# Kernel optimization log

Hardware: AMD Instinct MI355X
Metric: run time of the kernel (lower is better)

The kernel has to match this reference:

```python
import jax, jax.numpy as jnp
import numpy as np
from jax import lax

INPUT, HIDDEN, LAYERS = 256, 512, 3
SEQ, BATCH = 1024, 32
STDV = 1.0 / float(np.sqrt(HIDDEN))


def _uniform(key, shape):
    return jax.random.uniform(key, shape, jnp.float32, -STDV, STDV)


def setup_inputs() -> dict:
    key = jax.random.key(0)
    ks = iter(jax.random.split(key, 64))
    x = jax.random.normal(next(ks), (SEQ, BATCH, INPUT), jnp.float32)
    H3 = 3 * HIDDEN
    # layer 0: input dim = INPUT; layers 1..2: input dim = 2*HIDDEN
    w_ih_l0 = _uniform(next(ks), (2, H3, INPUT))          # (dir, 3H, in)
    w_hh_l0 = _uniform(next(ks), (2, H3, HIDDEN))
    b_ih_l0 = _uniform(next(ks), (2, H3))
    b_hh_l0 = _uniform(next(ks), (2, H3))
    w_ih_lr = _uniform(next(ks), (LAYERS - 1, 2, H3, 2 * HIDDEN))
    w_hh_lr = _uniform(next(ks), (LAYERS - 1, 2, H3, HIDDEN))
    b_ih_lr = _uniform(next(ks), (LAYERS - 1, 2, H3))
    b_hh_lr = _uniform(next(ks), (LAYERS - 1, 2, H3))
    return dict(x=x, w_ih_l0=w_ih_l0, w_hh_l0=w_hh_l0, b_ih_l0=b_ih_l0,
                b_hh_l0=b_hh_l0, w_ih_lr=w_ih_lr, w_hh_lr=w_hh_lr,
                b_ih_lr=b_ih_lr, b_hh_lr=b_hh_lr)


def _gru_dir(xs, w_ih, w_hh, b_ih, b_hh, reverse):
    # xs: (T, B, in); precompute input projection for the whole sequence
    Xi = jnp.einsum('tbi,gi->tbg', xs, w_ih) + b_ih  # (T, B, 3H)
    h0 = jnp.zeros((xs.shape[1], HIDDEN), xs.dtype)

    def step(h, xi):
        hp = h @ w_hh.T + b_hh                       # (B, 3H)
        ir, iz, inn = jnp.split(xi, 3, axis=-1)
        hr, hz, hn = jnp.split(hp, 3, axis=-1)
        r = jax.nn.sigmoid(ir + hr)
        z = jax.nn.sigmoid(iz + hz)
        n = jnp.tanh(inn + r * hn)
        h_new = (1.0 - z) * n + z * h
        return h_new, h_new

    h_last, ys = lax.scan(step, h0, Xi, reverse=reverse)
    return h_last, ys  # ys in original time order even when reverse=True


def reference(x, w_ih_l0, w_hh_l0, b_ih_l0, b_hh_l0,
              w_ih_lr, w_hh_lr, b_ih_lr, b_hh_lr):
    layer_input = x
    h_n = []
    for layer in range(LAYERS):
        if layer == 0:
            wi, wh, bi, bh = w_ih_l0, w_hh_l0, b_ih_l0, b_hh_l0
        else:
            wi, wh = w_ih_lr[layer - 1], w_hh_lr[layer - 1]
            bi, bh = b_ih_lr[layer - 1], b_hh_lr[layer - 1]
        hf, yf = _gru_dir(layer_input, wi[0], wh[0], bi[0], bh[0], reverse=False)
        hb, yb = _gru_dir(layer_input, wi[1], wh[1], bi[1], bh[1], reverse=True)
        h_n.append(hf)
        h_n.append(hb)
        layer_input = jnp.concatenate([yf, yb], axis=-1)  # (T, B, 2H)
    return jnp.stack(h_n, axis=0)  # (LAYERS*2, B, H)
```

## Files before the change

### kernel.cpp

```cpp
#include <hip/hip_runtime.h>
#include <stdint.h>

#define SEQ   1024
#define BATCH 32
#define HID   512
#define G3    1536
#define NW    32
#define JPW   16
#define THREADS 384
#define FSTR  256
#define CSTR  64
#define CH    16
#define NCH   64
#define NG    192
#define NPROD 192

typedef __attribute__((ext_vector_type(8))) short  short8;
typedef __attribute__((ext_vector_type(4))) float  f32x4;
typedef __attribute__((ext_vector_type(4))) unsigned short us4;
typedef unsigned long long ull;

__device__ __forceinline__ unsigned short f2bf(float f) {
  union { float f; unsigned int u; } v; v.f = f;
  unsigned int u = v.u;
  return (unsigned short)((u + 0x7FFFu + ((u >> 16) & 1u)) >> 16);
}
__device__ __forceinline__ float bf2f(unsigned short u) {
  union { unsigned int i; float f; } v; v.i = ((unsigned int)u) << 16; return v.f;
}
__device__ __forceinline__ short8 pack8(const float* __restrict__ p) {
  short8 o;
#pragma unroll
  for (int i = 0; i < 8; i++) o[i] = (short)f2bf(p[i]);
  return o;
}

__global__ void cvt_wb(const float* __restrict__ w, short8* __restrict__ out, int kcx, int nc) {
  int c = blockIdx.x * blockDim.x + threadIdx.x;
  if (c >= nc) return;
  int lane = c & 63, r = c >> 6;
  int kc = r % kcx, ng = r / kcx;
  int n   = ng * 16 + (lane & 15);
  int col = kc * 32 + (lane >> 4) * 8;
  int K = kcx * 32;
  out[c] = pack8(w + (size_t)n * K + col);
}

template<int KCX, bool WRITE_Y>
__global__ __launch_bounds__(THREADS, 1) void gru_mega(
    const void* __restrict__ Ain,
    short8* __restrict__ yout,
    const short8* __restrict__ wb,
    const float* __restrict__ whh,
    const float* __restrict__ bih,
    const float* __restrict__ bhh,
    us4* __restrict__ Xic,
    short8* __restrict__ hbuf,
    int* __restrict__ flags,
    int* __restrict__ prodcnt,
    float* __restrict__ hout)
{
  __shared__ float gbuf[4 * 512];
  __shared__ float hold[512];

  const int tid  = threadIdx.x;
  const int lane = tid & 63;
  const int wave = tid >> 6;
  const int quad = lane >> 4;
  const int l15  = lane & 15;

  if (blockIdx.x >= 64) {
    const int p    = blockIdx.x - 64;
    const int tg   = p & 15;
    const int ngg  = p >> 4;
    const int dirp = (ngg >= 6) ? 1 : 0;
    int* fl = flags + dirp * NW * FSTR;

    for (int c = 0; c < NCH; c++) {
      const int tgt = (c >= 2) ? CH * (c - 1) : 0;
      if (wave == 0) {
        while (true) {
          int v = (lane < NW)
                    ? __hip_atomic_load(&fl[lane * FSTR], __ATOMIC_RELAXED, __HIP_MEMORY_SCOPE_AGENT)
                    : tgt;
          if (__all(v >= tgt)) break;
          __builtin_amdgcn_s_sleep(4);
        }
      }
      __syncthreads();
      const int sl = tg;
      const int s  = c * CH + sl;
      const int t  = dirp ? (SEQ - 1 - s) : s;
      for (int mi = 0; mi < 2; mi++) {
        short8 a[KCX];
        if constexpr (KCX == 8) {
          const float* xr = (const float*)Ain + ((size_t)t * 32 + mi * 16 + l15) * 256 + quad * 8;
#pragma unroll
          for (int kc = 0; kc < KCX; kc++) a[kc] = pack8(xr + kc * 32);
        } else {
          const short8* ap = (const short8*)Ain + ((size_t)(t * 2 + mi) * KCX) * 64 + lane;
#pragma unroll
          for (int kc = 0; kc < KCX; kc++) a[kc] = ap[kc * 64];
        }
        for (int ng = ngg * 16 + wave; ng < ngg * 16 + 16; ng += 6) {
          const short8* bp = wb + (size_t)ng * KCX * 64 + lane;
          f32x4 ac0 = (f32x4){0.f, 0.f, 0.f, 0.f};
          f32x4 ac1 = (f32x4){0.f, 0.f, 0.f, 0.f};
#pragma unroll
          for (int kc = 0; kc < KCX; kc += 2) {
            ac0 = __builtin_amdgcn_mfma_f32_16x16x32_bf16(a[kc],     bp[kc * 64],       ac0, 0, 0, 0);
            ac1 = __builtin_amdgcn_mfma_f32_16x16x32_bf16(a[kc + 1], bp[(kc + 1) * 64], ac1, 0, 0, 0);
          }
          const int n  = ng * 16 + l15;
          const int gg = (ng % 96) >> 5;
          const float bias = bih[n] + (gg < 2 ? bhh[n] : 0.f);
          us4 o;
#pragma unroll
          for (int r = 0; r < 4; r++) o[r] = f2bf(ac0[r] + ac1[r] + bias);
          us4* dst = Xic + ((((size_t)(c & 1)) * CH + sl) * NG + ng) * 128 + mi * 64 + lane;
          asm volatile("global_store_dwordx2 %0, %1, off sc0 sc1" :: "v"(dst), "v"(o) : "memory");
        }
      }
      asm volatile("s_waitcnt vmcnt(0)" ::: "memory");
      __syncthreads();
      if (tid == 0)
        __hip_atomic_fetch_add(&prodcnt[c * CSTR], 1, __ATOMIC_RELAXED, __HIP_MEMORY_SCOPE_AGENT);
    }
    return;
  }

  const int mi  = wave & 1;
  const int g   = wave >> 1;
  const int dir = blockIdx.x >> 5;
  const int wg  = blockIdx.x & 31;
  const int j0  = wg * JPW;
  const bool rev = (dir == 1);
  const int ngR = dir * 96 + g * 32 + wg;

  short8 wh[16];
  {
    const float* pw = whh + (size_t)dir * G3 * HID + (size_t)(g * HID + j0 + l15) * HID + quad * 8;
#pragma unroll
    for (int kc = 0; kc < 16; kc++) wh[kc] = pack8(pw + kc * 32);
  }
  const float bh = bhh[dir * G3 + g * HID + j0 + l15];

  for (int idx = tid; idx < 512; idx += THREADS) hold[idx] = 0.f;
  __syncthreads();

  int* fl = flags + dir * NW * FSTR;
  char* hb = (char*)(hbuf + (size_t)dir * 2 * 2048);

  for (int s = 0; s < SEQ; s++) {
    const int t  = rev ? (SEQ - 1 - s) : s;
    const int c  = s >> 4;
    const int sl = s & 15;

    if (wave == 0) {
      while (true) {
        int v = (s > 0 && lane < NW)
                  ? __hip_atomic_load(&fl[lane * FSTR], __ATOMIC_RELAXED, __HIP_MEMORY_SCOPE_AGENT)
                  : s;
        bool ok = __all(v >= s);
        if (ok && sl == 0) {
          int cnt = __hip_atomic_load(&prodcnt[c * CSTR], __ATOMIC_RELAXED, __HIP_MEMORY_SCOPE_AGENT);
          ok = (cnt >= NPROD);
        }
        if (ok) break;
        __builtin_amdgcn_s_sleep(1);
      }
    }
    __syncthreads();

    const char* xp = (const char*)Xic
        + (((((size_t)(c & 1)) * CH + sl) * NG + ngR) * 128 + mi * 64 + lane) * 8;
    ull xi64;
    f32x4 p0 = (f32x4){0.f, 0.f, 0.f, 0.f};
    f32x4 p1 = (f32x4){0.f, 0.f, 0.f, 0.f};

    if (s > 0) {
      const char* hp = hb + (size_t)((s - 1) & 1) * 32768 + (size_t)mi * 16384 + (size_t)lane * 16;
      short8 a0, a1, a2, a3, a4, a5, a6, a7, a8, a9, a10, a11, a12, a13, a14, a15;
      asm volatile(
          "global_load_dwordx2 %16, %21, off sc0 sc1\n\t"
          "global_load_dwordx4 %0, %17, off sc0 sc1\n\t"
          "global_load_dwordx4 %1, %17, off offset:1024 sc0 sc1\n\t"
          "global_load_dwordx4 %2, %17, off offset:2048 sc0 sc1\n\t"
          "global_load_dwordx4 %3, %17, off offset:3072 sc0 sc1\n\t"
          "global_load_dwordx4 %4, %18, off sc0 sc1\n\t"
          "global_load_dwordx4 %5, %18, off offset:1024 sc0 sc1\n\t"
          "global_load_dwordx4 %6, %18, off offset:2048 sc0 sc1\n\t"
          "global_load_dwordx4 %7, %18, off offset:3072 sc0 sc1\n\t"
          "global_load_dwordx4 %8, %19, off sc0 sc1\n\t"
          "global_load_dwordx4 %9, %19, off offset:1024 sc0 sc1\n\t"
          "global_load_dwordx4 %10, %19, off offset:2048 sc0 sc1\n\t"
          "global_load_dwordx4 %11, %19, off offset:3072 sc0 sc1\n\t"
          "global_load_dwordx4 %12, %20, off sc0 sc1\n\t"
          "global_load_dwordx4 %13, %20, off offset:1024 sc0 sc1\n\t"
          "global_load_dwordx4 %14, %20, off offset:2048 sc0 sc1\n\t"
          "global_load_dwordx4 %15, %20, off offset:3072 sc0 sc1\n\t"
          "s_waitcnt vmcnt(0)"
          : "=&v"(a0), "=&v"(a1), "=&v"(a2), "=&v"(a3),
            "=&v"(a4), "=&v"(a5), "=&v"(a6), "=&v"(a7),
            "=&v"(a8), "=&v"(a9), "=&v"(a10), "=&v"(a11),
            "=&v"(a12), "=&v"(a13), "=&v"(a14), "=&v"(a15), "=&v"(xi64)
          : "v"(hp), "v"(hp + 4096), "v"(hp + 8192), "v"(hp + 12288), "v"(xp)
          : "memory");
      p0 = __builtin_amdgcn_mfma_f32_16x16x32_bf16(a0,  wh[0],  p0, 0, 0, 0);
      p1 = __builtin_amdgcn_mfma_f32_16x16x32_bf16(a1,  wh[1],  p1, 0, 0, 0);
      p0 = __builtin_amdgcn_mfma_f32_16x16x32_bf16(a2,  wh[2],  p0, 0, 0, 0);
      p1 = __builtin_amdgcn_mfma_f32_16x16x32_bf16(a3,  wh[3],  p1, 0, 0, 0);
      p0 = __builtin_amdgcn_mfma_f32_16x16x32_bf16(a4,  wh[4],  p0, 0, 0, 0);
      p1 = __builtin_amdgcn_mfma_f32_16x16x32_bf16(a5,  wh[5],  p1, 0, 0, 0);
      p0 = __builtin_amdgcn_mfma_f32_16x16x32_bf16(a6,  wh[6],  p0, 0, 0, 0);
      p1 = __builtin_amdgcn_mfma_f32_16x16x32_bf16(a7,  wh[7],  p1, 0, 0, 0);
      p0 = __builtin_amdgcn_mfma_f32_16x16x32_bf16(a8,  wh[8],  p0, 0, 0, 0);
      p1 = __builtin_amdgcn_mfma_f32_16x16x32_bf16(a9,  wh[9],  p1, 0, 0, 0);
      p0 = __builtin_amdgcn_mfma_f32_16x16x32_bf16(a10, wh[10], p0, 0, 0, 0);
      p1 = __builtin_amdgcn_mfma_f32_16x16x32_bf16(a11, wh[11], p1, 0, 0, 0);
      p0 = __builtin_amdgcn_mfma_f32_16x16x32_bf16(a12, wh[12], p0, 0, 0, 0);
      p1 = __builtin_amdgcn_mfma_f32_16x16x32_bf16(a13, wh[13], p1, 0, 0, 0);
      p0 = __builtin_amdgcn_mfma_f32_16x16x32_bf16(a14, wh[14], p0, 0, 0, 0);
      p1 = __builtin_amdgcn_mfma_f32_16x16x32_bf16(a15, wh[15], p1, 0, 0, 0);
    } else {
      asm volatile("global_load_dwordx2 %0, %1, off sc0 sc1\n\ts_waitcnt vmcnt(0)"
                   : "=&v"(xi64) : "v"(xp) : "memory");
    }

#pragma unroll
    for (int r = 0; r < 4; r++) {
      int m = mi * 16 + quad * 4 + r;
      float xv = bf2f((unsigned short)(xi64 >> (16 * r)));
      if (g < 2) {
        gbuf[(g * 32 + m) * JPW + l15] = xv + p0[r] + p1[r];
      } else {
        gbuf[(2 * 32 + m) * JPW + l15] = xv;
        gbuf[(3 * 32 + m) * JPW + l15] = bh + p0[r] + p1[r];
      }
    }
    __syncthreads();

    if (tid < 256) {
      int b = tid >> 3, jj = tid & 7;
      int e0 = b * 16 + 2 * jj;
      float h2[2];
#pragma unroll
      for (int e = 0; e < 2; e++) {
        int idx = e0 + e;
        int j = (idx & 15);
        float pr = gbuf[(0 * 32 + b) * JPW + j];
        float pz = gbuf[(1 * 32 + b) * JPW + j];
        float px = gbuf[(2 * 32 + b) * JPW + j];
        float ph = gbuf[(3 * 32 + b) * JPW + j];
        float rr = 1.f / (1.f + __expf(-pr));
        float zz = 1.f / (1.f + __expf(-pz));
        float a2 = px + rr * ph;
        float ex = __expf(2.f * a2);
        float nn = 1.f - 2.f / (ex + 1.f);
        float hp2 = hold[idx];
        float hnew = (1.f - zz) * nn + zz * hp2;
        hold[idx] = hnew;
        h2[e] = hnew;
      }
      unsigned int val = (unsigned int)f2bf(h2[0]) | ((unsigned int)f2bf(h2[1]) << 16);
      int k  = j0 + 2 * jj;
      int kc = k >> 5;
      int q  = (k >> 3) & 3;
      int l16 = (b & 15) + (q << 4);
      int mib = b >> 4;
      char* dst = hb + (size_t)(s & 1) * 32768 + (size_t)mib * 16384
                + (size_t)kc * 1024 + (size_t)l16 * 16 + (size_t)(k & 7) * 2;
      asm volatile("global_store_dword %0, %1, off sc0 sc1" :: "v"(dst), "v"(val) : "memory");
      if (WRITE_Y) {
        size_t yb = (((size_t)(t * 2 + mib) * 32 + (dir << 4) + kc) * 64 + l16) * 16 + (size_t)(k & 7) * 2;
        *(unsigned int*)((char*)yout + yb) = val;
      }
      if (s == SEQ - 1) {
        hout[((size_t)dir * 32 + b) * HID + k]     = h2[0];
        hout[((size_t)dir * 32 + b) * HID + k + 1] = h2[1];
      }
    }
    asm volatile("s_waitcnt vmcnt(0)" ::: "memory");
    __syncthreads();
    if (tid == 0)
      __hip_atomic_store(&fl[wg * FSTR], s + 1, __ATOMIC_RELAXED, __HIP_MEMORY_SCOPE_AGENT);
  }
}

extern "C" void kernel_launch(void* const* d_in, const int* in_sizes, int n_in,
                              void* d_out, int out_size, void* d_ws, size_t ws_size,
                              hipStream_t stream)
{
  const float* x       = (const float*)d_in[0];
  const float* w_ih_l0 = (const float*)d_in[1];
  const float* w_hh_l0 = (const float*)d_in[2];
  const float* b_ih_l0 = (const float*)d_in[3];
  const float* b_hh_l0 = (const float*)d_in[4];
  const float* w_ih_lr = (const float*)d_in[5];
  const float* w_hh_lr = (const float*)d_in[6];
  const float* b_ih_lr = (const float*)d_in[7];
  const float* b_hh_lr = (const float*)d_in[8];
  float* out = (float*)d_out;

  char* ws = (char*)d_ws;
  size_t off = 0;
  auto alloc = [&](size_t bytes) {
    char* p = ws + off;
    off += (bytes + 255) & ~(size_t)255;
    return p;
  };
  short8* y0   = (short8*)alloc((size_t)SEQ * 2 * 32 * 64 * 16);
  short8* y1   = (short8*)alloc((size_t)SEQ * 2 * 32 * 64 * 16);
  short8* wb   = (short8*)alloc((size_t)NG * 32 * 64 * 16);
  short8* hbuf = (short8*)alloc((size_t)2 * 2 * 2048 * 16);
  int*    flags   = (int*)alloc((size_t)3 * 2 * NW * FSTR * 4);
  int*    prodcnt = (int*)alloc((size_t)3 * NCH * CSTR * 4);
  us4*    Xic  = (us4*)alloc((size_t)2 * CH * NG * 2 * 64 * 8);

  hipMemsetAsync(flags, 0, (size_t)3 * 2 * NW * FSTR * 4, stream);
  hipMemsetAsync(prodcnt, 0, (size_t)3 * NCH * CSTR * 4, stream);

  {
    int nc = NG * 8 * 64;
    cvt_wb<<<(nc + 255) / 256, 256, 0, stream>>>(w_ih_l0, wb, 8, nc);
    gru_mega<8, true><<<256, THREADS, 0, stream>>>(
        x, y0, wb, w_hh_l0, b_ih_l0, b_hh_l0, Xic, hbuf, flags, prodcnt, out);
  }
  {
    int nc = NG * 32 * 64;
    cvt_wb<<<(nc + 255) / 256, 256, 0, stream>>>(w_ih_lr, wb, 32, nc);
    gru_mega<32, true><<<256, THREADS, 0, stream>>>(
        y0, y1, wb, w_hh_lr, b_ih_lr, b_hh_lr, Xic, hbuf,
        flags + 2 * NW * FSTR, prodcnt + NCH * CSTR, out + 2 * BATCH * HID);
  }
  {
    int nc = NG * 32 * 64;
    cvt_wb<<<(nc + 255) / 256, 256, 0, stream>>>(w_ih_lr + (size_t)2 * G3 * 1024, wb, 32, nc);
    gru_mega<32, false><<<256, THREADS, 0, stream>>>(
        y1, nullptr, wb, w_hh_lr + (size_t)2 * G3 * HID,
        b_ih_lr + 2 * G3, b_hh_lr + 2 * G3, Xic, hbuf,
        flags + 4 * NW * FSTR, prodcnt + 2 * NCH * CSTR, out + 4 * BATCH * HID);
  }
}
```

Before: 9.948 ms.

## Replace per-step flag polling with tag bits embedded in hidden-state data

The recurrent consumer blocks no longer poll per-workgroup flags and barrier before each step. Instead they spin on the hidden-state loads, checking a parity tag packed into the low bit of each bf16 element. Producer blocks are re-split so each handles 4 gate tiles and keeps their weights in LDS. The h write becomes one 16-byte store per thread, gbuf is padded to avoid bank conflicts, and the sc0 cache bits are dropped. The tag bit perturbs the lowest mantissa bit of one bf16 value per 8, and correctness now depends on the 0xFF-initialised buffers and on memory ordering without an explicit handshake.

```diff
diff --git a/kernel.cpp b/kernel.cpp
--- a/kernel.cpp
+++ b/kernel.cpp
@@ -6,7 +6,6 @@
 #define HID   512
 #define G3    1536
 #define NW    32
-#define JPW   16
 #define THREADS 384
 #define FSTR  256
 #define CSTR  64
@@ -14,6 +13,7 @@
 #define NCH   64
 #define NG    192
 #define NPROD 192
+#define GS    17
 
 typedef __attribute__((ext_vector_type(8))) short  short8;
 typedef __attribute__((ext_vector_type(4))) float  f32x4;
@@ -60,8 +60,9 @@
     int* __restrict__ prodcnt,
     float* __restrict__ hout)
 {
-  __shared__ float gbuf[4 * 512];
-  __shared__ float hold[512];
+  extern __shared__ short8 wlds[];
+  __shared__ float gbuf[4 * 32 * GS];
+  __shared__ float hold[32 * GS];
 
   const int tid  = threadIdx.x;
   const int lane = tid & 63;
@@ -71,10 +72,15 @@
 
   if (blockIdx.x >= 64) {
     const int p    = blockIdx.x - 64;
-    const int tg   = p & 15;
-    const int ngg  = p >> 4;
-    const int dirp = (ngg >= 6) ? 1 : 0;
+    const int ngq  = p >> 2;
+    const int tg   = p & 3;
+    const int dirp = (ngq >= 24) ? 1 : 0;
+    const int ng0  = ngq * 4;
     int* fl = flags + dirp * NW * FSTR;
+
+    for (int idx = tid; idx < 4 * KCX * 64; idx += THREADS)
+      wlds[idx] = wb[(size_t)ng0 * KCX * 64 + idx];
+    __syncthreads();
 
     for (int c = 0; c < NCH; c++) {
       const int tgt = (c >= 2) ? CH * (c - 1) : 0;
@@ -88,22 +94,24 @@
         }
       }
       __syncthreads();
-      const int sl = tg;
-      const int s  = c * CH + sl;
-      const int t  = dirp ? (SEQ - 1 - s) : s;
-      for (int mi = 0; mi < 2; mi++) {
-        short8 a[KCX];
-        if constexpr (KCX == 8) {
-          const float* xr = (const float*)Ain + ((size_t)t * 32 + mi * 16 + l15) * 256 + quad * 8;
-#pragma unroll
-          for (int kc = 0; kc < KCX; kc++) a[kc] = pack8(xr + kc * 32);
-        } else {
-          const short8* ap = (const short8*)Ain + ((size_t)(t * 2 + mi) * KCX) * 64 + lane;
-#pragma unroll
-          for (int kc = 0; kc < KCX; kc++) a[kc] = ap[kc * 64];
-        }
-        for (int ng = ngg * 16 + wave; ng < ngg * 16 + 16; ng += 6) {
-          const short8* bp = wb + (size_t)ng * KCX * 64 + lane;
+      for (int i = 0; i < 4; i++) {
+        const int sl = i * 4 + tg;
+        const int s  = c * CH + sl;
+        const int t  = dirp ? (SEQ - 1 - s) : s;
+        for (int task = wave; task < 8; task += 6) {
+          const int mi = task & 1;
+          const int ng = task >> 1;
+          short8 a[KCX];
+          if constexpr (KCX == 8) {
+            const float* xr = (const float*)Ain + ((size_t)t * 32 + mi * 16 + l15) * 256 + quad * 8;
+#pragma unroll
+            for (int kc = 0; kc < KCX; kc++) a[kc] = pack8(xr + kc * 32);
+          } else {
+            const short8* ap = (const short8*)Ain + ((size_t)(t * 2 + mi) * KCX) * 64 + lane;
+#pragma unroll
+            for (int kc = 0; kc < KCX; kc++) a[kc] = ap[kc * 64];
+          }
+          const short8* bp = wlds + ng * (KCX * 64) + lane;
           f32x4 ac0 = (f32x4){0.f, 0.f, 0.f, 0.f};
           f32x4 ac1 = (f32x4){0.f, 0.f, 0.f, 0.f};
 #pragma unroll
@@ -111,14 +119,15 @@
             ac0 = __builtin_amdgcn_mfma_f32_16x16x32_bf16(a[kc],     bp[kc * 64],       ac0, 0, 0, 0);
             ac1 = __builtin_amdgcn_mfma_f32_16x16x32_bf16(a[kc + 1], bp[(kc + 1) * 64], ac1, 0, 0, 0);
           }
-          const int n  = ng * 16 + l15;
-          const int gg = (ng % 96) >> 5;
+          const int ngg = ng0 + ng;
+          const int n   = ngg * 16 + l15;
+          const int gg  = (ngg % 96) >> 5;
           const float bias = bih[n] + (gg < 2 ? bhh[n] : 0.f);
           us4 o;
 #pragma unroll
           for (int r = 0; r < 4; r++) o[r] = f2bf(ac0[r] + ac1[r] + bias);
-          us4* dst = Xic + ((((size_t)(c & 1)) * CH + sl) * NG + ng) * 128 + mi * 64 + lane;
-          asm volatile("global_store_dwordx2 %0, %1, off sc0 sc1" :: "v"(dst), "v"(o) : "memory");
+          us4* dst = Xic + (((size_t)(c & 1) * CH + sl) * NG + ngg) * 128 + mi * 64 + lane;
+          asm volatile("global_store_dwordx2 %0, %1, off sc1" :: "v"(dst), "v"(o) : "memory");
         }
       }
       asm volatile("s_waitcnt vmcnt(0)" ::: "memory");
@@ -133,7 +142,7 @@
   const int g   = wave >> 1;
   const int dir = blockIdx.x >> 5;
   const int wg  = blockIdx.x & 31;
-  const int j0  = wg * JPW;
+  const int j0  = wg * 16;
   const bool rev = (dir == 1);
   const int ngR = dir * 96 + g * 32 + wg;
 
@@ -145,7 +154,7 @@
   }
   const float bh = bhh[dir * G3 + g * HID + j0 + l15];
 
-  for (int idx = tid; idx < 512; idx += THREADS) hold[idx] = 0.f;
+  for (int idx = tid; idx < 32 * GS; idx += THREADS) hold[idx] = 0.f;
   __syncthreads();
 
   int* fl = flags + dir * NW * FSTR;
@@ -156,56 +165,57 @@
     const int c  = s >> 4;
     const int sl = s & 15;
 
-    if (wave == 0) {
-      while (true) {
-        int v = (s > 0 && lane < NW)
-                  ? __hip_atomic_load(&fl[lane * FSTR], __ATOMIC_RELAXED, __HIP_MEMORY_SCOPE_AGENT)
-                  : s;
-        bool ok = __all(v >= s);
-        if (ok && sl == 0) {
-          int cnt = __hip_atomic_load(&prodcnt[c * CSTR], __ATOMIC_RELAXED, __HIP_MEMORY_SCOPE_AGENT);
-          ok = (cnt >= NPROD);
-        }
-        if (ok) break;
+    if (sl == 0) {
+      while (__hip_atomic_load(&prodcnt[c * CSTR], __ATOMIC_RELAXED, __HIP_MEMORY_SCOPE_AGENT) < NPROD)
         __builtin_amdgcn_s_sleep(1);
-      }
-    }
-    __syncthreads();
+    }
 
     const char* xp = (const char*)Xic
-        + (((((size_t)(c & 1)) * CH + sl) * NG + ngR) * 128 + mi * 64 + lane) * 8;
+        + ((((size_t)(c & 1) * CH + sl) * NG + ngR) * 128 + mi * 64 + lane) * 8;
     ull xi64;
     f32x4 p0 = (f32x4){0.f, 0.f, 0.f, 0.f};
     f32x4 p1 = (f32x4){0.f, 0.f, 0.f, 0.f};
 
     if (s > 0) {
       const char* hp = hb + (size_t)((s - 1) & 1) * 32768 + (size_t)mi * 16384 + (size_t)lane * 16;
+      const int tag = ((s - 1) >> 1) & 1;
       short8 a0, a1, a2, a3, a4, a5, a6, a7, a8, a9, a10, a11, a12, a13, a14, a15;
-      asm volatile(
-          "global_load_dwordx2 %16, %21, off sc0 sc1\n\t"
-          "global_load_dwordx4 %0, %17, off sc0 sc1\n\t"
-          "global_load_dwordx4 %1, %17, off offset:1024 sc0 sc1\n\t"
-          "global_load_dwordx4 %2, %17, off offset:2048 sc0 sc1\n\t"
-          "global_load_dwordx4 %3, %17, off offset:3072 sc0 sc1\n\t"
-          "global_load_dwordx4 %4, %18, off sc0 sc1\n\t"
-          "global_load_dwordx4 %5, %18, off offset:1024 sc0 sc1\n\t"
-          "global_load_dwordx4 %6, %18, off offset:2048 sc0 sc1\n\t"
-          "global_load_dwordx4 %7, %18, off offset:3072 sc0 sc1\n\t"
-          "global_load_dwordx4 %8, %19, off sc0 sc1\n\t"
-          "global_load_dwordx4 %9, %19, off offset:1024 sc0 sc1\n\t"
-          "global_load_dwordx4 %10, %19, off offset:2048 sc0 sc1\n\t"
-          "global_load_dwordx4 %11, %19, off offset:3072 sc0 sc1\n\t"
-          "global_load_dwordx4 %12, %20, off sc0 sc1\n\t"
-          "global_load_dwordx4 %13, %20, off offset:1024 sc0 sc1\n\t"
-          "global_load_dwordx4 %14, %20, off offset:2048 sc0 sc1\n\t"
-          "global_load_dwordx4 %15, %20, off offset:3072 sc0 sc1\n\t"
-          "s_waitcnt vmcnt(0)"
-          : "=&v"(a0), "=&v"(a1), "=&v"(a2), "=&v"(a3),
-            "=&v"(a4), "=&v"(a5), "=&v"(a6), "=&v"(a7),
-            "=&v"(a8), "=&v"(a9), "=&v"(a10), "=&v"(a11),
-            "=&v"(a12), "=&v"(a13), "=&v"(a14), "=&v"(a15), "=&v"(xi64)
-          : "v"(hp), "v"(hp + 4096), "v"(hp + 8192), "v"(hp + 12288), "v"(xp)
-          : "memory");
+      while (true) {
+        asm volatile(
+            "global_load_dwordx2 %16, %21, off sc1\n\t"
+            "global_load_dwordx4 %0, %17, off sc1\n\t"
+            "global_load_dwordx4 %1, %17, off offset:1024 sc1\n\t"
+            "global_load_dwordx4 %2, %17, off offset:2048 sc1\n\t"
+            "global_load_dwordx4 %3, %17, off offset:3072 sc1\n\t"
+            "global_load_dwordx4 %4, %18, off sc1\n\t"
+            "global_load_dwordx4 %5, %18, off offset:1024 sc1\n\t"
+            "global_load_dwordx4 %6, %18, off offset:2048 sc1\n\t"
+            "global_load_dwordx4 %7, %18, off offset:3072 sc1\n\t"
+            "global_load_dwordx4 %8, %19, off sc1\n\t"
+            "global_load_dwordx4 %9, %19, off offset:1024 sc1\n\t"
+            "global_load_dwordx4 %10, %19, off offset:2048 sc1\n\t"
+            "global_load_dwordx4 %11, %19, off offset:3072 sc1\n\t"
+            "global_load_dwordx4 %12, %20, off sc1\n\t"
+            "global_load_dwordx4 %13, %20, off offset:1024 sc1\n\t"
+            "global_load_dwordx4 %14, %20, off offset:2048 sc1\n\t"
+            "global_load_dwordx4 %15, %20, off offset:3072 sc1\n\t"
+            "s_waitcnt vmcnt(0)"
+            : "=&v"(a0), "=&v"(a1), "=&v"(a2), "=&v"(a3),
+              "=&v"(a4), "=&v"(a5), "=&v"(a6), "=&v"(a7),
+              "=&v"(a8), "=&v"(a9), "=&v"(a10), "=&v"(a11),
+              "=&v"(a12), "=&v"(a13), "=&v"(a14), "=&v"(a15), "=&v"(xi64)
+            : "v"(hp), "v"(hp + 4096), "v"(hp + 8192), "v"(hp + 12288), "v"(xp)
+            : "memory");
+        bool ok = ((a0[7]  & 1) == tag) & ((a1[7]  & 1) == tag)
+                & ((a2[7]  & 1) == tag) & ((a3[7]  & 1) == tag)
+                & ((a4[7]  & 1) == tag) & ((a5[7]  & 1) == tag)
+                & ((a6[7]  & 1) == tag) & ((a7[7]  & 1) == tag)
+                & ((a8[7]  & 1) == tag) & ((a9[7]  & 1) == tag)
+                & ((a10[7] & 1) == tag) & ((a11[7] & 1) == tag)
+                & ((a12[7] & 1) == tag) & ((a13[7] & 1) == tag)
+                & ((a14[7] & 1) == tag) & ((a15[7] & 1) == tag);
+        if (__all(ok)) break;
+      }
       p0 = __builtin_amdgcn_mfma_f32_16x16x32_bf16(a0,  wh[0],  p0, 0, 0, 0);
       p1 = __builtin_amdgcn_mfma_f32_16x16x32_bf16(a1,  wh[1],  p1, 0, 0, 0);
       p0 = __builtin_amdgcn_mfma_f32_16x16x32_bf16(a2,  wh[2],  p0, 0, 0, 0);
@@ -223,7 +233,7 @@
       p0 = __builtin_amdgcn_mfma_f32_16x16x32_bf16(a14, wh[14], p0, 0, 0, 0);
       p1 = __builtin_amdgcn_mfma_f32_16x16x32_bf16(a15, wh[15], p1, 0, 0, 0);
     } else {
-      asm volatile("global_load_dwordx2 %0, %1, off sc0 sc1\n\ts_waitcnt vmcnt(0)"
+      asm volatile("global_load_dwordx2 %0, %1, off sc1\n\ts_waitcnt vmcnt(0)"
                    : "=&v"(xi64) : "v"(xp) : "memory");
     }
 
@@ -232,58 +242,56 @@
       int m = mi * 16 + quad * 4 + r;
       float xv = bf2f((unsigned short)(xi64 >> (16 * r)));
       if (g < 2) {
-        gbuf[(g * 32 + m) * JPW + l15] = xv + p0[r] + p1[r];
+        gbuf[(g * 32 + m) * GS + l15] = xv + p0[r] + p1[r];
       } else {
-        gbuf[(2 * 32 + m) * JPW + l15] = xv;
-        gbuf[(3 * 32 + m) * JPW + l15] = bh + p0[r] + p1[r];
+        gbuf[(2 * 32 + m) * GS + l15] = xv;
+        gbuf[(3 * 32 + m) * GS + l15] = bh + p0[r] + p1[r];
       }
     }
     __syncthreads();
 
-    if (tid < 256) {
-      int b = tid >> 3, jj = tid & 7;
-      int e0 = b * 16 + 2 * jj;
-      float h2[2];
-#pragma unroll
-      for (int e = 0; e < 2; e++) {
-        int idx = e0 + e;
-        int j = (idx & 15);
-        float pr = gbuf[(0 * 32 + b) * JPW + j];
-        float pz = gbuf[(1 * 32 + b) * JPW + j];
-        float px = gbuf[(2 * 32 + b) * JPW + j];
-        float ph = gbuf[(3 * 32 + b) * JPW + j];
+    if (tid < 64) {
+      const int b     = tid >> 1;
+      const int khalf = tid & 1;
+      short8 val;
+      float hv[8];
+#pragma unroll
+      for (int jj = 0; jj < 8; jj++) {
+        int j = khalf * 8 + jj;
+        float pr = gbuf[(0 * 32 + b) * GS + j];
+        float pz = gbuf[(1 * 32 + b) * GS + j];
+        float px = gbuf[(2 * 32 + b) * GS + j];
+        float ph = gbuf[(3 * 32 + b) * GS + j];
         float rr = 1.f / (1.f + __expf(-pr));
         float zz = 1.f / (1.f + __expf(-pz));
         float a2 = px + rr * ph;
         float ex = __expf(2.f * a2);
         float nn = 1.f - 2.f / (ex + 1.f);
-        float hp2 = hold[idx];
+        float hp2 = hold[b * GS + j];
         float hnew = (1.f - zz) * nn + zz * hp2;
-        hold[idx] = hnew;
-        h2[e] = hnew;
-      }
-      unsigned int val = (unsigned int)f2bf(h2[0]) | ((unsigned int)f2bf(h2[1]) << 16);
-      int k  = j0 + 2 * jj;
-      int kc = k >> 5;
-      int q  = (k >> 3) & 3;
-      int l16 = (b & 15) + (q << 4);
-      int mib = b >> 4;
+        hold[b * GS + j] = hnew;
+        hv[jj] = hnew;
+        val[jj] = (short)f2bf(hnew);
+      }
+      val[7] = (short)((val[7] & ~1) | ((s >> 1) & 1));
+      const int k8  = wg * 2 + khalf;
+      const int kc  = k8 >> 2;
+      const int qd  = k8 & 3;
+      const int mib = b >> 4;
+      const int lnb = b & 15;
       char* dst = hb + (size_t)(s & 1) * 32768 + (size_t)mib * 16384
-                + (size_t)kc * 1024 + (size_t)l16 * 16 + (size_t)(k & 7) * 2;
-      asm volatile("global_store_dword %0, %1, off sc0 sc1" :: "v"(dst), "v"(val) : "memory");
-      if (WRITE_Y) {
-        size_t yb = (((size_t)(t * 2 + mib) * 32 + (dir << 4) + kc) * 64 + l16) * 16 + (size_t)(k & 7) * 2;
-        *(unsigned int*)((char*)yout + yb) = val;
-      }
+                + (size_t)kc * 1024 + (size_t)(qd * 16 + lnb) * 16;
+      asm volatile("global_store_dwordx4 %0, %1, off sc1" :: "v"(dst), "v"(val) : "memory");
+      if (WRITE_Y)
+        yout[((size_t)(t * 2 + mib) * 32 + (dir << 4) + kc) * 64 + qd * 16 + lnb] = val;
       if (s == SEQ - 1) {
-        hout[((size_t)dir * 32 + b) * HID + k]     = h2[0];
-        hout[((size_t)dir * 32 + b) * HID + k + 1] = h2[1];
-      }
-    }
-    asm volatile("s_waitcnt vmcnt(0)" ::: "memory");
-    __syncthreads();
-    if (tid == 0)
-      __hip_atomic_store(&fl[wg * FSTR], s + 1, __ATOMIC_RELAXED, __HIP_MEMORY_SCOPE_AGENT);
+#pragma unroll
+        for (int jj = 0; jj < 8; jj++)
+          hout[((size_t)dir * 32 + b) * HID + j0 + khalf * 8 + jj] = hv[jj];
+      }
+      if (tid == 0)
+        __hip_atomic_store(&fl[wg * FSTR], s + 1, __ATOMIC_RELAXED, __HIP_MEMORY_SCOPE_AGENT);
+    }
   }
 }
 
@@ -312,33 +320,43 @@
   short8* y0   = (short8*)alloc((size_t)SEQ * 2 * 32 * 64 * 16);
   short8* y1   = (short8*)alloc((size_t)SEQ * 2 * 32 * 64 * 16);
   short8* wb   = (short8*)alloc((size_t)NG * 32 * 64 * 16);
-  short8* hbuf = (short8*)alloc((size_t)2 * 2 * 2048 * 16);
+  short8* hbuf = (short8*)alloc((size_t)3 * 2 * 2 * 2048 * 16);
   int*    flags   = (int*)alloc((size_t)3 * 2 * NW * FSTR * 4);
   int*    prodcnt = (int*)alloc((size_t)3 * NCH * CSTR * 4);
   us4*    Xic  = (us4*)alloc((size_t)2 * CH * NG * 2 * 64 * 8);
 
   hipMemsetAsync(flags, 0, (size_t)3 * 2 * NW * FSTR * 4, stream);
   hipMemsetAsync(prodcnt, 0, (size_t)3 * NCH * CSTR * 4, stream);
+  hipMemsetAsync(hbuf, 0xFF, (size_t)3 * 2 * 2 * 2048 * 16, stream);
+
+  const int smem0 = 4 * 8  * 64 * 16;
+  const int smem1 = 4 * 32 * 64 * 16;
+  hipFuncSetAttribute(reinterpret_cast<const void*>(gru_mega<8, true>),
+                      hipFuncAttributeMaxDynamicSharedMemorySize, smem0);
+  hipFuncSetAttribute(reinterpret_cast<const void*>(gru_mega<32, true>),
+                      hipFuncAttributeMaxDynamicSharedMemorySize, smem1);
+  hipFuncSetAttribute(reinterpret_cast<const void*>(gru_mega<32, false>),
+                      hipFuncAttributeMaxDynamicSharedMemorySize, smem1);
 
   {
     int nc = NG * 8 * 64;
     cvt_wb<<<(nc + 255) / 256, 256, 0, stream>>>(w_ih_l0, wb, 8, nc);
-    gru_mega<8, true><<<256, THREADS, 0, stream>>>(
+    gru_mega<8, true><<<256, THREADS, smem0, stream>>>(
         x, y0, wb, w_hh_l0, b_ih_l0, b_hh_l0, Xic, hbuf, flags, prodcnt, out);
   }
   {
     int nc = NG * 32 * 64;
     cvt_wb<<<(nc + 255) / 256, 256, 0, stream>>>(w_ih_lr, wb, 32, nc);
-    gru_mega<32, true><<<256, THREADS, 0, stream>>>(
-        y0, y1, wb, w_hh_lr, b_ih_lr, b_hh_lr, Xic, hbuf,
+    gru_mega<32, true><<<256, THREADS, smem1, stream>>>(
+        y0, y1, wb, w_hh_lr, b_ih_lr, b_hh_lr, Xic, hbuf + 8192,
         flags + 2 * NW * FSTR, prodcnt + NCH * CSTR, out + 2 * BATCH * HID);
   }
   {
     int nc = NG * 32 * 64;
     cvt_wb<<<(nc + 255) / 256, 256, 0, stream>>>(w_ih_lr + (size_t)2 * G3 * 1024, wb, 32, nc);
-    gru_mega<32, false><<<256, THREADS, 0, stream>>>(
+    gru_mega<32, false><<<256, THREADS, smem1, stream>>>(
         y1, nullptr, wb, w_hh_lr + (size_t)2 * G3 * HID,
-        b_ih_lr + 2 * G3, b_hh_lr + 2 * G3, Xic, hbuf,
+        b_ih_lr + 2 * G3, b_hh_lr + 2 * G3, Xic, hbuf + 16384,
         flags + 4 * NW * FSTR, prodcnt + 2 * NCH * CSTR, out + 4 * BATCH * HID);
   }
 }
```

Result: slower. 11.46 ms (+15.2%).
